# Kernel tuning notes

Hardware: AMD Instinct MI355X
Metric: run time of the kernel (lower is better)

The kernel has to match this reference:

```python
import jax, jax.numpy as jnp
import numpy as np

# T-MAC weight-only quantized linear, mathematically-equivalent reference.
# Weights: ternary {-1,0,1} via per-tensor scale s_w = 1/mean|W| (pesudo_tmac_weight_quant,
# force_per_tensor=True). Dequant scale = 1/s_w.
# Activations: the LUT preprocessing quantizes per act_group_size=64 group to uint8 with
# per-group LUT_Scales/LUT_Biases; equivalent math is symmetric int8 per-group quantization.
# qgemm_lut accumulates LUT entries indexed by weight bits == qW @ x_hat, then applies scales.

ACT_GROUP = 64  # op_config.act_group_size


def setup_inputs() -> dict:
    key = jax.random.key(0)
    k1, k2 = jax.random.split(key)
    N, M, K = 8, 8192, 8192
    x = jax.random.normal(k1, (N, K), dtype=jnp.float32)
    weight = jax.random.normal(k2, (M, K), dtype=jnp.float32) * 0.02
    return {"x": x, "weight": weight}


def reference(x, weight):
    M, K = weight.shape
    N = x.shape[0]
    # --- weight ternary quantization (per-tensor) ---
    s_w = 1.0 / jnp.clip(jnp.mean(jnp.abs(weight)), 1e-5, None)
    qW = jnp.clip(jnp.round(weight * s_w), -1.0, 1.0)  # [M, K] in {-1,0,1}
    w_deq = 1.0 / s_w  # per-tensor dequant scale (weight_scales)
    # --- activation per-group int8 quantization (LUT precision emulation) ---
    xg = x.reshape(N, K // ACT_GROUP, ACT_GROUP)
    a_scale = jnp.maximum(jnp.max(jnp.abs(xg), axis=-1, keepdims=True) / 127.0, 1e-8)
    x_hat = (jnp.round(xg / a_scale) * a_scale).reshape(N, K)
    # --- lookup-accumulate GEMM == dense GEMM with quantized operands ---
    y = jnp.einsum('nk,mk->nm', x_hat, qW) * w_deq  # [N, M]
    return y.astype(x.dtype)
```

## Files before the change

### kernel.cpp

```cpp
#include <hip/hip_runtime.h>
#include <math.h>

#define K_DIM 8192
#define M_DIM 8192
#define N_DIM 8
#define RED_BLOCKS 2048

__global__ __launch_bounds__(256) void k_abssum(const float4* __restrict__ W4,
                                                double* __restrict__ partials,
                                                int n4) {
    int tid = blockIdx.x * blockDim.x + threadIdx.x;
    int stride = gridDim.x * blockDim.x;
    float s0 = 0.f, s1 = 0.f, s2 = 0.f, s3 = 0.f;
    for (int i = tid; i < n4; i += stride) {
        float4 v = W4[i];
        s0 += fabsf(v.x); s1 += fabsf(v.y);
        s2 += fabsf(v.z); s3 += fabsf(v.w);
    }
    float s = (s0 + s1) + (s2 + s3);
    #pragma unroll
    for (int off = 32; off > 0; off >>= 1) s += __shfl_xor(s, off, 64);
    __shared__ float sm[4];
    if ((threadIdx.x & 63) == 0) sm[threadIdx.x >> 6] = s;
    __syncthreads();
    if (threadIdx.x == 0) {
        double t = ((double)sm[0] + (double)sm[1]) +
                   ((double)sm[2] + (double)sm[3]);
        partials[blockIdx.x] = t;
    }
}

__global__ __launch_bounds__(256) void k_final(const double* __restrict__ partials,
                                               int nparts,
                                               float* __restrict__ scal) {
    double s = 0.0;
    for (int i = threadIdx.x; i < nparts; i += 256) s += partials[i];
    #pragma unroll
    for (int off = 32; off > 0; off >>= 1) s += __shfl_xor(s, off, 64);
    __shared__ double sm[4];
    if ((threadIdx.x & 63) == 0) sm[threadIdx.x >> 6] = s;
    __syncthreads();
    if (threadIdx.x == 0) {
        double tot = (sm[0] + sm[1]) + (sm[2] + sm[3]);
        float meanf = (float)(tot / (double)((long long)M_DIM * K_DIM));
        float clipped = fmaxf(meanf, 1e-5f);
        float s_w = 1.0f / clipped;
        float w_deq = 1.0f / s_w;
        scal[0] = s_w;
        scal[1] = w_deq;
    }
}

__global__ __launch_bounds__(256) void k_actq(const float* __restrict__ x,
                                              float* __restrict__ xh) {
    int idx = blockIdx.x * blockDim.x + threadIdx.x;
    float v = x[idx];
    float a = fabsf(v);
    #pragma unroll
    for (int off = 32; off > 0; off >>= 1) a = fmaxf(a, __shfl_xor(a, off, 64));
    float scale = fmaxf(a / 127.0f, 1e-8f);
    float q = rintf(v / scale);
    xh[idx] = q * scale;
}

__device__ __forceinline__ float quant1(float w, float s_w) {
    return fminf(1.0f, fmaxf(-1.0f, rintf(w * s_w)));
}

__global__ __launch_bounds__(256) void k_gemm(const float* __restrict__ W,
                                              const float* __restrict__ xh,
                                              const float* __restrict__ scal,
                                              float* __restrict__ out) {
    const float s_w   = scal[0];
    const float w_deq = scal[1];
    const int wave = threadIdx.x >> 6;
    const int lane = threadIdx.x & 63;
    const int m0 = blockIdx.x * 8 + wave * 2;

    const float* Wr0 = W + (size_t)(m0 + 0) * K_DIM;
    const float* Wr1 = W + (size_t)(m0 + 1) * K_DIM;

    float acc[2][8];
    #pragma unroll
    for (int r = 0; r < 2; ++r)
        #pragma unroll
        for (int n = 0; n < 8; ++n) acc[r][n] = 0.0f;

    #pragma unroll 2
    for (int it = 0; it < K_DIM / 256; ++it) {
        const int k = it * 256 + lane * 4;
        float4 w0 = *(const float4*)(Wr0 + k);
        float4 w1 = *(const float4*)(Wr1 + k);
        float4 xv[8];
        #pragma unroll
        for (int n = 0; n < 8; ++n)
            xv[n] = *(const float4*)(xh + n * K_DIM + k);

        float4 q0, q1;
        q0.x = quant1(w0.x, s_w); q0.y = quant1(w0.y, s_w);
        q0.z = quant1(w0.z, s_w); q0.w = quant1(w0.w, s_w);
        q1.x = quant1(w1.x, s_w); q1.y = quant1(w1.y, s_w);
        q1.z = quant1(w1.z, s_w); q1.w = quant1(w1.w, s_w);

        #pragma unroll
        for (int n = 0; n < 8; ++n) {
            acc[0][n] = fmaf(q0.x, xv[n].x, acc[0][n]);
            acc[0][n] = fmaf(q0.y, xv[n].y, acc[0][n]);
            acc[0][n] = fmaf(q0.z, xv[n].z, acc[0][n]);
            acc[0][n] = fmaf(q0.w, xv[n].w, acc[0][n]);
            acc[1][n] = fmaf(q1.x, xv[n].x, acc[1][n]);
            acc[1][n] = fmaf(q1.y, xv[n].y, acc[1][n]);
            acc[1][n] = fmaf(q1.z, xv[n].z, acc[1][n]);
            acc[1][n] = fmaf(q1.w, xv[n].w, acc[1][n]);
        }
    }

    #pragma unroll
    for (int r = 0; r < 2; ++r) {
        #pragma unroll
        for (int n = 0; n < 8; ++n) {
            float v = acc[r][n];
            #pragma unroll
            for (int off = 32; off > 0; off >>= 1) v += __shfl_xor(v, off, 64);
            acc[r][n] = v;
        }
    }
    if (lane == 0) {
        #pragma unroll
        for (int r = 0; r < 2; ++r)
            #pragma unroll
            for (int n = 0; n < 8; ++n)
                out[n * M_DIM + (m0 + r)] = w_deq * acc[r][n];
    }
}

extern "C" void kernel_launch(void* const* d_in, const int* in_sizes, int n_in,
                              void* d_out, int out_size, void* d_ws, size_t ws_size,
                              hipStream_t stream) {
    const float* x = (const float*)d_in[0];
    const float* W = (const float*)d_in[1];
    float* out = (float*)d_out;

    double* partials = (double*)d_ws;
    float* scal = (float*)((char*)d_ws + 16384);
    float* xh = (float*)((char*)d_ws + 32768);

    const int n4 = (M_DIM * K_DIM) / 4;

    k_abssum<<<RED_BLOCKS, 256, 0, stream>>>((const float4*)W, partials, n4);
    k_actq<<<(N_DIM * K_DIM) / 256, 256, 0, stream>>>(x, xh);
    k_final<<<1, 256, 0, stream>>>(partials, RED_BLOCKS, scal);
    k_gemm<<<M_DIM / 8, 256, 0, stream>>>(W, xh, scal, out);
}
```

Baseline: 415.3 us.

## Fuse preprocessing kernels and fold final reduction into GEMM blocks

Merges the weight abs-sum reduction and activation quantization into one launch, and drops the single-block final-reduce kernel by having every GEMM block re-reduce the 2048 partials itself. It also software-prefetches the next weight float4s in the GEMM loop and adds a launch-bounds occupancy hint. This removes two kernel launches and the serial single-block step, at the cost of redundant partial reads in each of the 1024 GEMM blocks.

```diff
diff --git a/kernel.cpp b/kernel.cpp
--- a/kernel.cpp
+++ b/kernel.cpp
@@ -5,74 +5,97 @@
 #define M_DIM 8192
 #define N_DIM 8
 #define RED_BLOCKS 2048
+#define ACTQ_BLOCKS 256
 
-__global__ __launch_bounds__(256) void k_abssum(const float4* __restrict__ W4,
-                                                double* __restrict__ partials,
-                                                int n4) {
-    int tid = blockIdx.x * blockDim.x + threadIdx.x;
-    int stride = gridDim.x * blockDim.x;
-    float s0 = 0.f, s1 = 0.f, s2 = 0.f, s3 = 0.f;
-    for (int i = tid; i < n4; i += stride) {
-        float4 v = W4[i];
-        s0 += fabsf(v.x); s1 += fabsf(v.y);
-        s2 += fabsf(v.z); s3 += fabsf(v.w);
+__global__ __launch_bounds__(256) void k_pre(const float4* __restrict__ W4,
+                                             double* __restrict__ partials,
+                                             const float* __restrict__ x,
+                                             float* __restrict__ xh,
+                                             int n4) {
+    if (blockIdx.x < RED_BLOCKS) {
+        int tid = blockIdx.x * 256 + threadIdx.x;
+        const int stride = RED_BLOCKS * 256;
+        float s0 = 0.f, s1 = 0.f, s2 = 0.f, s3 = 0.f;
+        for (int i = tid; i < n4; i += stride) {
+            float4 v = W4[i];
+            s0 += fabsf(v.x); s1 += fabsf(v.y);
+            s2 += fabsf(v.z); s3 += fabsf(v.w);
+        }
+        float s = (s0 + s1) + (s2 + s3);
+        #pragma unroll
+        for (int off = 32; off > 0; off >>= 1) s += __shfl_xor(s, off, 64);
+        __shared__ float sm[4];
+        if ((threadIdx.x & 63) == 0) sm[threadIdx.x >> 6] = s;
+        __syncthreads();
+        if (threadIdx.x == 0) {
+            double t = ((double)sm[0] + (double)sm[1]) +
+                       ((double)sm[2] + (double)sm[3]);
+            partials[blockIdx.x] = t;
+        }
+    } else {
+        int idx = (blockIdx.x - RED_BLOCKS) * 256 + threadIdx.x;
+        float v = x[idx];
+        float a = fabsf(v);
+        #pragma unroll
+        for (int off = 32; off > 0; off >>= 1) a = fmaxf(a, __shfl_xor(a, off, 64));
+        float scale = fmaxf(a / 127.0f, 1e-8f);
+        float q = rintf(v / scale);
+        xh[idx] = q * scale;
     }
-    float s = (s0 + s1) + (s2 + s3);
-    #pragma unroll
-    for (int off = 32; off > 0; off >>= 1) s += __shfl_xor(s, off, 64);
-    __shared__ float sm[4];
-    if ((threadIdx.x & 63) == 0) sm[threadIdx.x >> 6] = s;
-    __syncthreads();
-    if (threadIdx.x == 0) {
-        double t = ((double)sm[0] + (double)sm[1]) +
-                   ((double)sm[2] + (double)sm[3]);
-        partials[blockIdx.x] = t;
-    }
-}
-
-__global__ __launch_bounds__(256) void k_final(const double* __restrict__ partials,
-                                               int nparts,
-                                               float* __restrict__ scal) {
-    double s = 0.0;
-    for (int i = threadIdx.x; i < nparts; i += 256) s += partials[i];
-    #pragma unroll
-    for (int off = 32; off > 0; off >>= 1) s += __shfl_xor(s, off, 64);
-    __shared__ double sm[4];
-    if ((threadIdx.x & 63) == 0) sm[threadIdx.x >> 6] = s;
-    __syncthreads();
-    if (threadIdx.x == 0) {
-        double tot = (sm[0] + sm[1]) + (sm[2] + sm[3]);
-        float meanf = (float)(tot / (double)((long long)M_DIM * K_DIM));
-        float clipped = fmaxf(meanf, 1e-5f);
-        float s_w = 1.0f / clipped;
-        float w_deq = 1.0f / s_w;
-        scal[0] = s_w;
-        scal[1] = w_deq;
-    }
-}
-
-__global__ __launch_bounds__(256) void k_actq(const float* __restrict__ x,
-                                              float* __restrict__ xh) {
-    int idx = blockIdx.x * blockDim.x + threadIdx.x;
-    float v = x[idx];
-    float a = fabsf(v);
-    #pragma unroll
-    for (int off = 32; off > 0; off >>= 1) a = fmaxf(a, __shfl_xor(a, off, 64));
-    float scale = fmaxf(a / 127.0f, 1e-8f);
-    float q = rintf(v / scale);
-    xh[idx] = q * scale;
 }
 
 __device__ __forceinline__ float quant1(float w, float s_w) {
     return fminf(1.0f, fmaxf(-1.0f, rintf(w * s_w)));
 }
 
-__global__ __launch_bounds__(256) void k_gemm(const float* __restrict__ W,
-                                              const float* __restrict__ xh,
-                                              const float* __restrict__ scal,
-                                              float* __restrict__ out) {
-    const float s_w   = scal[0];
-    const float w_deq = scal[1];
+__device__ __forceinline__ void fma_step(float acc[2][8],
+                                         const float4& w0, const float4& w1,
+                                         const float4 xv[8], float s_w) {
+    float4 q0, q1;
+    q0.x = quant1(w0.x, s_w); q0.y = quant1(w0.y, s_w);
+    q0.z = quant1(w0.z, s_w); q0.w = quant1(w0.w, s_w);
+    q1.x = quant1(w1.x, s_w); q1.y = quant1(w1.y, s_w);
+    q1.z = quant1(w1.z, s_w); q1.w = quant1(w1.w, s_w);
+    #pragma unroll
+    for (int n = 0; n < 8; ++n) {
+        acc[0][n] = fmaf(q0.x, xv[n].x, acc[0][n]);
+        acc[0][n] = fmaf(q0.y, xv[n].y, acc[0][n]);
+        acc[0][n] = fmaf(q0.z, xv[n].z, acc[0][n]);
+        acc[0][n] = fmaf(q0.w, xv[n].w, acc[0][n]);
+        acc[1][n] = fmaf(q1.x, xv[n].x, acc[1][n]);
+        acc[1][n] = fmaf(q1.y, xv[n].y, acc[1][n]);
+        acc[1][n] = fmaf(q1.z, xv[n].z, acc[1][n]);
+        acc[1][n] = fmaf(q1.w, xv[n].w, acc[1][n]);
+    }
+}
+
+__global__ __launch_bounds__(256, 4) void k_gemm(const float* __restrict__ W,
+                                                 const float* __restrict__ xh,
+                                                 const double* __restrict__ partials,
+                                                 float* __restrict__ out) {
+    __shared__ double smd[4];
+    __shared__ float s_scal[2];
+    {
+        double s = 0.0;
+        for (int i = threadIdx.x; i < RED_BLOCKS; i += 256) s += partials[i];
+        #pragma unroll
+        for (int off = 32; off > 0; off >>= 1) s += __shfl_xor(s, off, 64);
+        if ((threadIdx.x & 63) == 0) smd[threadIdx.x >> 6] = s;
+        __syncthreads();
+        if (threadIdx.x == 0) {
+            double tot = (smd[0] + smd[1]) + (smd[2] + smd[3]);
+            float meanf = (float)(tot / (double)((long long)M_DIM * K_DIM));
+            float clipped = fmaxf(meanf, 1e-5f);
+            float s_w = 1.0f / clipped;
+            float w_deq = 1.0f / s_w;
+            s_scal[0] = s_w;
+            s_scal[1] = w_deq;
+        }
+        __syncthreads();
+    }
+    const float s_w   = s_scal[0];
+    const float w_deq = s_scal[1];
+
     const int wave = threadIdx.x >> 6;
     const int lane = threadIdx.x & 63;
     const int m0 = blockIdx.x * 8 + wave * 2;
@@ -86,33 +109,29 @@
         #pragma unroll
         for (int n = 0; n < 8; ++n) acc[r][n] = 0.0f;
 
+    float4 w0c = *(const float4*)(Wr0 + lane * 4);
+    float4 w1c = *(const float4*)(Wr1 + lane * 4);
+
     #pragma unroll 2
-    for (int it = 0; it < K_DIM / 256; ++it) {
-        const int k = it * 256 + lane * 4;
-        float4 w0 = *(const float4*)(Wr0 + k);
-        float4 w1 = *(const float4*)(Wr1 + k);
+    for (int it = 0; it < K_DIM / 256 - 1; ++it) {
+        const int k  = it * 256 + lane * 4;
+        const int kn = k + 256;
+        float4 w0 = w0c, w1 = w1c;
+        w0c = *(const float4*)(Wr0 + kn);
+        w1c = *(const float4*)(Wr1 + kn);
         float4 xv[8];
         #pragma unroll
         for (int n = 0; n < 8; ++n)
             xv[n] = *(const float4*)(xh + n * K_DIM + k);
-
-        float4 q0, q1;
-        q0.x = quant1(w0.x, s_w); q0.y = quant1(w0.y, s_w);
-        q0.z = quant1(w0.z, s_w); q0.w = quant1(w0.w, s_w);
-        q1.x = quant1(w1.x, s_w); q1.y = quant1(w1.y, s_w);
-        q1.z = quant1(w1.z, s_w); q1.w = quant1(w1.w, s_w);
-
+        fma_step(acc, w0, w1, xv, s_w);
+    }
+    {
+        const int k = (K_DIM / 256 - 1) * 256 + lane * 4;
+        float4 xv[8];
         #pragma unroll
-        for (int n = 0; n < 8; ++n) {
-            acc[0][n] = fmaf(q0.x, xv[n].x, acc[0][n]);
-            acc[0][n] = fmaf(q0.y, xv[n].y, acc[0][n]);
-            acc[0][n] = fmaf(q0.z, xv[n].z, acc[0][n]);
-            acc[0][n] = fmaf(q0.w, xv[n].w, acc[0][n]);
-            acc[1][n] = fmaf(q1.x, xv[n].x, acc[1][n]);
-            acc[1][n] = fmaf(q1.y, xv[n].y, acc[1][n]);
-            acc[1][n] = fmaf(q1.z, xv[n].z, acc[1][n]);
-            acc[1][n] = fmaf(q1.w, xv[n].w, acc[1][n]);
-        }
+        for (int n = 0; n < 8; ++n)
+            xv[n] = *(const float4*)(xh + n * K_DIM + k);
+        fma_step(acc, w0c, w1c, xv, s_w);
     }
 
     #pragma unroll
@@ -142,13 +161,11 @@
     float* out = (float*)d_out;
 
     double* partials = (double*)d_ws;
-    float* scal = (float*)((char*)d_ws + 16384);
     float* xh = (float*)((char*)d_ws + 32768);
 
     const int n4 = (M_DIM * K_DIM) / 4;
 
-    k_abssum<<<RED_BLOCKS, 256, 0, stream>>>((const float4*)W, partials, n4);
-    k_actq<<<(N_DIM * K_DIM) / 256, 256, 0, stream>>>(x, xh);
-    k_final<<<1, 256, 0, stream>>>(partials, RED_BLOCKS, scal);
-    k_gemm<<<M_DIM / 8, 256, 0, stream>>>(W, xh, scal, out);
+    k_pre<<<RED_BLOCKS + ACTQ_BLOCKS, 256, 0, stream>>>((const float4*)W,
+                                                        partials, x, xh, n4);
+    k_gemm<<<M_DIM / 8, 256, 0, stream>>>(W, xh, partials, out);
 }
```

After: 410.8 us. About the same (-1.1%).
